# Kernel tuning notes

Hardware: AMD Instinct MI355X
Metric: run time of the kernel (lower is better)

## Reference

```python
import jax, jax.numpy as jnp
import numpy as np

N = 100000
E = 1600000
IN_DIM = 256
HID = 64


def setup_inputs() -> dict:
    key = jax.random.key(0)
    k1, k2, k3 = jax.random.split(key, 3)
    x = jax.random.normal(k1, (N, IN_DIM), dtype=jnp.float32)
    edge_index = jax.random.randint(k2, (2, E), 0, N, dtype=jnp.int64)
    # glorot-ish init for GCNConv weight, zero bias (PyG default)
    W = jax.random.normal(k3, (IN_DIM, HID), dtype=jnp.float32) * (1.0 / np.sqrt(IN_DIM))
    b = jnp.zeros((HID,), dtype=jnp.float32)
    return {"x": x, "edge_index": edge_index, "W": W, "b": b}


def reference(x, edge_index, W, b):
    # GCNConv: out = D^{-1/2} (A + I) D^{-1/2} (X W) + b
    n = x.shape[0]
    # add self-loops
    loop = jnp.arange(n, dtype=edge_index.dtype)
    src = jnp.concatenate([edge_index[0], loop])  # [E+N]
    dst = jnp.concatenate([edge_index[1], loop])  # [E+N]
    # degree of target nodes (incl. self-loops)
    deg = jax.ops.segment_sum(jnp.ones_like(dst, dtype=x.dtype), dst, num_segments=n)
    dinv = jnp.where(deg > 0, jax.lax.rsqrt(deg), 0.0)  # deg^{-1/2}, inf->0
    norm = dinv[src] * dinv[dst]  # [E+N]
    h = x @ W  # [N, HID] transform before aggregation
    msg = h[src] * norm[:, None]  # gather + scale, [E+N, HID]
    out = jax.ops.segment_sum(msg, dst, num_segments=n)  # scatter-add
    return out + b
```

## Files before the change

kernel.cpp:

```cpp
#include <hip/hip_runtime.h>

typedef float floatx4 __attribute__((ext_vector_type(4)));
typedef short s16x8 __attribute__((ext_vector_type(8)));

#define WG 256
#define NBUCK 512
#define BSH 8
#define EBLK 512
#define CAP 8192

__device__ inline unsigned pack_bf16_rne(float a, float b) {
    unsigned ua = __float_as_uint(a), ub = __float_as_uint(b);
    ua = (ua + 0x7FFFu + ((ua >> 16) & 1u)) >> 16;
    ub = (ub + 0x7FFFu + ((ub >> 16) & 1u)) >> 16;
    return ua | (ub << 16);
}

union FragU {
    unsigned u[4];
    uint4 q;
    s16x8 v;
};

__global__ __launch_bounds__(WG) void k_build(const void* __restrict__ ei, int* __restrict__ cursor,
                                              unsigned* __restrict__ ebuf, int E) {
    __shared__ int h[NBUCK];
    __shared__ int base[NBUCK];
    __shared__ int s32flag;
    const int t = threadIdx.x;
    if (t == 0) s32flag = 0;
    for (int i = t; i < NBUCK; i += WG) h[i] = 0;
    __syncthreads();
    {
        const int* w = (const int*)ei;
        int nz = 0;
        for (int j = t; j < 4096; j += WG) nz |= (w[2 * j + 1] != 0);
        if (nz) atomicOr(&s32flag, 1);
    }
    __syncthreads();
    const bool i32 = (s32flag != 0);
    const int chunk = (E + EBLK - 1) / EBLK;
    const int s = blockIdx.x * chunk;
    const int eend = min(E, s + chunk);
    if (i32) {
        const int* pd = (const int*)ei + E;
        for (int e = s + t; e < eend; e += WG) atomicAdd(&h[pd[e] >> BSH], 1);
    } else {
        const long long* pd = (const long long*)ei + E;
        for (int e = s + t; e < eend; e += WG) atomicAdd(&h[(int)pd[e] >> BSH], 1);
    }
    __syncthreads();
    for (int i = t; i < NBUCK; i += WG) {
        int c = h[i];
        base[i] = c ? atomicAdd(&cursor[i], c) : 0;
        h[i] = 0;
    }
    __syncthreads();
    for (int e = s + t; e < eend; e += WG) {
        int sN, dN;
        if (i32) {
            const int* p = (const int*)ei;
            sN = p[e];
            dN = p[E + e];
        } else {
            const long long* p = (const long long*)ei;
            sN = (int)p[e];
            dN = (int)p[(long long)E + e];
        }
        int bkt = dN >> BSH;
        int pos = base[bkt] + atomicAdd(&h[bkt], 1);
        if (pos < CAP) ebuf[(size_t)bkt * CAP + pos] = (unsigned)sN | ((unsigned)(dN & 255) << 24);
    }
}

__global__ __launch_bounds__(WG) void k_mid(const unsigned* __restrict__ ebuf, const int* __restrict__ cursor,
                                            int* __restrict__ off, int* __restrict__ srcs,
                                            float* __restrict__ dinv,
                                            const float* __restrict__ x, const float* __restrict__ W,
                                            unsigned short* __restrict__ g, int N, int nbuse) {
    __shared__ unsigned smem[2048 * 4];
    const int t = threadIdx.x;

    if ((int)blockIdx.x < nbuse) {
        int* red = (int*)smem;
        int* h = red + 256;
        int* sc = h + 256;
        int* cur = sc + 256;
        const int b = blockIdx.x;
        const int node0 = b << BSH;
        const int rows = min(256, N - node0);
        int part = 0;
        for (int i = t; i < b; i += WG) part += min(cursor[i], CAP);
        red[t] = part;
        h[t] = 0;
        __syncthreads();
        for (int d = WG / 2; d > 0; d >>= 1) {
            if (t < d) red[t] += red[t + d];
            __syncthreads();
        }
        const int ebase = red[0];
        const int cnt = min(cursor[b], CAP);
        const unsigned* eb = ebuf + (size_t)b * CAP;
        for (int j = t; j < cnt; j += WG) atomicAdd(&h[eb[j] >> 24], 1);
        __syncthreads();
        const int deg = (t < rows) ? h[t] + 1 : 0;
        sc[t] = deg;
        __syncthreads();
        for (int d = 1; d < 256; d <<= 1) {
            int a = (t >= d) ? sc[t - d] : 0;
            __syncthreads();
            sc[t] += a;
            __syncthreads();
        }
        const int basef = ebase + node0;
        const int local = sc[t] - deg;
        if (t < rows) {
            off[node0 + t] = basef + local;
            srcs[basef + local] = node0 + t;
            cur[t] = local + 1;
            dinv[node0 + t] = rsqrtf((float)deg);
        }
        if (b == nbuse - 1 && t == 0) off[N] = ebase + cnt + N;
        __syncthreads();
        for (int j = t; j < cnt; j += WG) {
            unsigned w = eb[j];
            int dl = (int)(w >> 24);
            int pos = basef + atomicAdd(&cur[dl], 1);
            srcs[pos] = (int)(w & 0xFFFFFFu);
        }
    } else {
        const int bb = blockIdx.x - nbuse;
        for (int q = t; q < 2048; q += WG) {
            const int kb = q >> 8, nt = (q >> 6) & 3, ln = q & 63;
            const int quad = ln >> 4, l15 = ln & 15;
            const int col = nt * 16 + l15;
            const int krow = kb * 32 + quad * 8;
            unsigned up[4];
#pragma unroll
            for (int p = 0; p < 4; p++) {
                float a = W[(krow + 2 * p) * 64 + col];
                float b2 = W[(krow + 2 * p + 1) * 64 + col];
                up[p] = pack_bf16_rne(a, b2);
            }
            uint4 pk = {up[0], up[1], up[2], up[3]};
            *(uint4*)(&smem[q * 4]) = pk;
        }
        __syncthreads();

        const int wv = t >> 6;
        const int lane = t & 63;
        const int quad = lane >> 4, l15 = lane & 15;

        long long arow = (long long)bb * 64 + wv * 16 + l15;
        if (arow >= N) arow = N - 1;
        const float* xr = x + arow * 256 + quad * 8;

        floatx4 xv[8][2];
#pragma unroll
        for (int kb = 0; kb < 8; kb++) {
            xv[kb][0] = *(const floatx4*)(xr + kb * 32);
            xv[kb][1] = *(const floatx4*)(xr + kb * 32 + 4);
        }

        floatx4 acc[4];
#pragma unroll
        for (int nt = 0; nt < 4; nt++) acc[nt] = 0.f;

#pragma unroll
        for (int kb = 0; kb < 8; kb++) {
            FragU a;
            a.u[0] = pack_bf16_rne(xv[kb][0][0], xv[kb][0][1]);
            a.u[1] = pack_bf16_rne(xv[kb][0][2], xv[kb][0][3]);
            a.u[2] = pack_bf16_rne(xv[kb][1][0], xv[kb][1][1]);
            a.u[3] = pack_bf16_rne(xv[kb][1][2], xv[kb][1][3]);
#pragma unroll
            for (int nt = 0; nt < 4; nt++) {
                FragU b2;
                b2.q = *(const uint4*)(&smem[((kb * 4 + nt) * 64 + lane) * 4]);
                acc[nt] = __builtin_amdgcn_mfma_f32_16x16x32_bf16(a.v, b2.v, acc[nt], 0, 0, 0);
            }
        }

        const long long orow0 = (long long)bb * 64 + wv * 16 + quad * 4;
#pragma unroll
        for (int r = 0; r < 4; r++) {
            const long long orow = orow0 + r;
            if (orow < N) {
#pragma unroll
                for (int nt = 0; nt < 4; nt++) {
                    float v = acc[nt][r];
                    unsigned uv = __float_as_uint(v);
                    uv = (uv + 0x7FFFu + ((uv >> 16) & 1u)) >> 16;
                    g[orow * 64 + nt * 16 + l15] = (unsigned short)uv;
                }
            }
        }
    }
}

__global__ __launch_bounds__(WG) void k_gather(const unsigned short* __restrict__ g,
                                               const int* __restrict__ off, const int* __restrict__ srcs,
                                               const float* __restrict__ dinv, const float* __restrict__ bias,
                                               float* __restrict__ out, int N) {
    int wid = (blockIdx.x * WG + threadIdx.x) >> 6;
    int lane = threadIdx.x & 63;
    if (wid >= N) return;
    int grp = lane >> 3;
    int c8 = (lane & 7) * 8;
    int e0 = off[wid], e1 = off[wid + 1];
    float a0 = 0.f, a1 = 0.f, a2 = 0.f, a3 = 0.f, a4 = 0.f, a5 = 0.f, a6 = 0.f, a7 = 0.f;
    int e = e0 + grp;
    int s = (e < e1) ? srcs[e] : 0;
    while (e < e1) {
        int en = e + 8;
        int sn = (en < e1) ? srcs[en] : 0;
        float ds = dinv[s];
        uint4 v = *(const uint4*)(g + (long long)s * 64 + c8);
        a0 += ds * __uint_as_float(v.x << 16);
        a1 += ds * __uint_as_float(v.x & 0xFFFF0000u);
        a2 += ds * __uint_as_float(v.y << 16);
        a3 += ds * __uint_as_float(v.y & 0xFFFF0000u);
        a4 += ds * __uint_as_float(v.z << 16);
        a5 += ds * __uint_as_float(v.z & 0xFFFF0000u);
        a6 += ds * __uint_as_float(v.w << 16);
        a7 += ds * __uint_as_float(v.w & 0xFFFF0000u);
        s = sn;
        e = en;
    }
#pragma unroll
    for (int m = 8; m <= 32; m <<= 1) {
        a0 += __shfl_xor(a0, m, 64);
        a1 += __shfl_xor(a1, m, 64);
        a2 += __shfl_xor(a2, m, 64);
        a3 += __shfl_xor(a3, m, 64);
        a4 += __shfl_xor(a4, m, 64);
        a5 += __shfl_xor(a5, m, 64);
        a6 += __shfl_xor(a6, m, 64);
        a7 += __shfl_xor(a7, m, 64);
    }
    if (grp == 0) {
        float d = dinv[wid];
        const floatx4 b0 = *(const floatx4*)(bias + c8);
        const floatx4 b1 = *(const floatx4*)(bias + c8 + 4);
        floatx4 o0, o1;
        o0[0] = d * a0 + b0[0];
        o0[1] = d * a1 + b0[1];
        o0[2] = d * a2 + b0[2];
        o0[3] = d * a3 + b0[3];
        o1[0] = d * a4 + b1[0];
        o1[1] = d * a5 + b1[1];
        o1[2] = d * a6 + b1[2];
        o1[3] = d * a7 + b1[3];
        *(floatx4*)(out + (long long)wid * 64 + c8) = o0;
        *(floatx4*)(out + (long long)wid * 64 + c8 + 4) = o1;
    }
}

extern "C" void kernel_launch(void* const* d_in, const int* in_sizes, int n_in,
                              void* d_out, int out_size, void* d_ws, size_t ws_size,
                              hipStream_t stream) {
    const float* x = (const float*)d_in[0];
    const void* ei = d_in[1];
    const float* W = (const float*)d_in[2];
    const float* b = (const float*)d_in[3];
    float* out = (float*)d_out;

    const int N = in_sizes[0] / 256;
    const int E = in_sizes[1] / 2;
    const int NBUSE = (N + 255) >> BSH;
    const int GEMMB = (N + 63) / 64;

    char* ws = (char*)d_ws;
    size_t o = 0;
    auto alloc = [&](size_t bytes) -> void* {
        void* p = ws + o;
        o += (bytes + 255) & ~(size_t)255;
        return p;
    };
    float* dinv = (float*)alloc((size_t)N * 4);
    unsigned short* g = (unsigned short*)alloc((size_t)N * 64 * 2);
    unsigned* ebuf = (unsigned*)alloc((size_t)NBUSE * CAP * 4);
    int* cursor = (int*)alloc((size_t)NBUCK * 4);
    int* off = (int*)alloc((size_t)(N + 1) * 4);
    int* srcs = (int*)alloc((size_t)(E + N) * 4);
    if (o > ws_size) return;

    hipMemsetAsync(cursor, 0, (size_t)NBUCK * 4, stream);
    k_build<<<EBLK, WG, 0, stream>>>(ei, cursor, ebuf, E);
    k_mid<<<NBUSE + GEMMB, WG, 0, stream>>>(ebuf, cursor, off, srcs, dinv, x, W, g, N, NBUSE);
    k_gather<<<(N * 64 + WG - 1) / WG, WG, 0, stream>>>(g, off, srcs, dinv, b, out, N);
}
```

Measured before the change: 269.3 us.

## Overlap edge bucketing with GEMM in one launch and pre-pack W once

```diff
diff --git a/kernel.cpp b/kernel.cpp
--- a/kernel.cpp
+++ b/kernel.cpp
@@ -16,134 +16,100 @@
     return ua | (ub << 16);
 }
 
+__device__ inline float bf_lo(unsigned u) { return __uint_as_float(u << 16); }
+__device__ inline float bf_hi(unsigned u) { return __uint_as_float(u & 0xFFFF0000u); }
+
 union FragU {
     unsigned u[4];
     uint4 q;
     s16x8 v;
 };
 
-__global__ __launch_bounds__(WG) void k_build(const void* __restrict__ ei, int* __restrict__ cursor,
-                                              unsigned* __restrict__ ebuf, int E) {
-    __shared__ int h[NBUCK];
-    __shared__ int base[NBUCK];
-    __shared__ int s32flag;
-    const int t = threadIdx.x;
-    if (t == 0) s32flag = 0;
-    for (int i = t; i < NBUCK; i += WG) h[i] = 0;
-    __syncthreads();
-    {
-        const int* w = (const int*)ei;
-        int nz = 0;
-        for (int j = t; j < 4096; j += WG) nz |= (w[2 * j + 1] != 0);
-        if (nz) atomicOr(&s32flag, 1);
-    }
-    __syncthreads();
-    const bool i32 = (s32flag != 0);
-    const int chunk = (E + EBLK - 1) / EBLK;
-    const int s = blockIdx.x * chunk;
-    const int eend = min(E, s + chunk);
-    if (i32) {
-        const int* pd = (const int*)ei + E;
-        for (int e = s + t; e < eend; e += WG) atomicAdd(&h[pd[e] >> BSH], 1);
-    } else {
-        const long long* pd = (const long long*)ei + E;
-        for (int e = s + t; e < eend; e += WG) atomicAdd(&h[(int)pd[e] >> BSH], 1);
-    }
-    __syncthreads();
-    for (int i = t; i < NBUCK; i += WG) {
-        int c = h[i];
-        base[i] = c ? atomicAdd(&cursor[i], c) : 0;
-        h[i] = 0;
-    }
-    __syncthreads();
-    for (int e = s + t; e < eend; e += WG) {
-        int sN, dN;
-        if (i32) {
-            const int* p = (const int*)ei;
-            sN = p[e];
-            dN = p[E + e];
-        } else {
-            const long long* p = (const long long*)ei;
-            sN = (int)p[e];
-            dN = (int)p[(long long)E + e];
-        }
-        int bkt = dN >> BSH;
-        int pos = base[bkt] + atomicAdd(&h[bkt], 1);
-        if (pos < CAP) ebuf[(size_t)bkt * CAP + pos] = (unsigned)sN | ((unsigned)(dN & 255) << 24);
-    }
-}
-
-__global__ __launch_bounds__(WG) void k_mid(const unsigned* __restrict__ ebuf, const int* __restrict__ cursor,
-                                            int* __restrict__ off, int* __restrict__ srcs,
-                                            float* __restrict__ dinv,
-                                            const float* __restrict__ x, const float* __restrict__ W,
-                                            unsigned short* __restrict__ g, int N, int nbuse) {
+__global__ __launch_bounds__(WG) void k_prep(const float* __restrict__ W, unsigned* __restrict__ Wf,
+                                             int* __restrict__ cursor) {
+    if (blockIdx.x == 0) {
+        if (threadIdx.x < NBUCK / 2) *(int2*)(cursor + threadIdx.x * 2) = {0, 0};
+    }
+    const int q = blockIdx.x * WG + threadIdx.x;
+    const int kb = q >> 8, nt = (q >> 6) & 3, ln = q & 63;
+    const int quad = ln >> 4, l15 = ln & 15;
+    const int col = nt * 16 + l15;
+    const int krow = kb * 32 + quad * 8;
+    unsigned up[4];
+#pragma unroll
+    for (int p = 0; p < 4; p++) {
+        float a = W[(krow + 2 * p) * 64 + col];
+        float b = W[(krow + 2 * p + 1) * 64 + col];
+        up[p] = pack_bf16_rne(a, b);
+    }
+    uint4 pk = {up[0], up[1], up[2], up[3]};
+    *(uint4*)(&Wf[q * 4]) = pk;
+}
+
+__global__ __launch_bounds__(WG) void k_bg(const void* __restrict__ ei, int* __restrict__ cursor,
+                                           unsigned* __restrict__ ebuf,
+                                           const float* __restrict__ x, const unsigned* __restrict__ Wf,
+                                           unsigned short* __restrict__ g, int N, int E) {
     __shared__ unsigned smem[2048 * 4];
     const int t = threadIdx.x;
-
-    if ((int)blockIdx.x < nbuse) {
-        int* red = (int*)smem;
-        int* h = red + 256;
-        int* sc = h + 256;
-        int* cur = sc + 256;
-        const int b = blockIdx.x;
-        const int node0 = b << BSH;
-        const int rows = min(256, N - node0);
-        int part = 0;
-        for (int i = t; i < b; i += WG) part += min(cursor[i], CAP);
-        red[t] = part;
-        h[t] = 0;
-        __syncthreads();
-        for (int d = WG / 2; d > 0; d >>= 1) {
-            if (t < d) red[t] += red[t + d];
-            __syncthreads();
-        }
-        const int ebase = red[0];
-        const int cnt = min(cursor[b], CAP);
-        const unsigned* eb = ebuf + (size_t)b * CAP;
-        for (int j = t; j < cnt; j += WG) atomicAdd(&h[eb[j] >> 24], 1);
-        __syncthreads();
-        const int deg = (t < rows) ? h[t] + 1 : 0;
-        sc[t] = deg;
-        __syncthreads();
-        for (int d = 1; d < 256; d <<= 1) {
-            int a = (t >= d) ? sc[t - d] : 0;
-            __syncthreads();
-            sc[t] += a;
-            __syncthreads();
-        }
-        const int basef = ebase + node0;
-        const int local = sc[t] - deg;
-        if (t < rows) {
-            off[node0 + t] = basef + local;
-            srcs[basef + local] = node0 + t;
-            cur[t] = local + 1;
-            dinv[node0 + t] = rsqrtf((float)deg);
-        }
-        if (b == nbuse - 1 && t == 0) off[N] = ebase + cnt + N;
-        __syncthreads();
-        for (int j = t; j < cnt; j += WG) {
-            unsigned w = eb[j];
-            int dl = (int)(w >> 24);
-            int pos = basef + atomicAdd(&cur[dl], 1);
-            srcs[pos] = (int)(w & 0xFFFFFFu);
+    const int b = blockIdx.x;
+    const bool isBuild = ((b & 3) == 0) && ((b >> 2) < EBLK);
+
+    if (isBuild) {
+        int* h = (int*)smem;
+        int* base = h + NBUCK;
+        int* s32flag = base + NBUCK;
+        const int bid = b >> 2;
+        if (t == 0) *s32flag = 0;
+        for (int i = t; i < NBUCK; i += WG) h[i] = 0;
+        __syncthreads();
+        {
+            const int* w = (const int*)ei;
+            int nz = 0;
+            for (int j = t; j < 4096; j += WG) nz |= (w[2 * j + 1] != 0);
+            if (nz) atomicOr(s32flag, 1);
+        }
+        __syncthreads();
+        const bool i32 = (*s32flag != 0);
+        const int chunk = (E + EBLK - 1) / EBLK;
+        const int s = bid * chunk;
+        const int eend = min(E, s + chunk);
+        if (i32) {
+            const int* pd = (const int*)ei + E;
+            for (int e = s + t; e < eend; e += WG) atomicAdd(&h[pd[e] >> BSH], 1);
+        } else {
+            const long long* pd = (const long long*)ei + E;
+            for (int e = s + t; e < eend; e += WG) atomicAdd(&h[(int)pd[e] >> BSH], 1);
+        }
+        __syncthreads();
+        for (int i = t; i < NBUCK; i += WG) {
+            int c = h[i];
+            base[i] = c ? atomicAdd(&cursor[i], c) : 0;
+            h[i] = 0;
+        }
+        __syncthreads();
+        for (int e = s + t; e < eend; e += WG) {
+            int sN, dN;
+            if (i32) {
+                const int* p = (const int*)ei;
+                sN = p[e];
+                dN = p[E + e];
+            } else {
+                const long long* p = (const long long*)ei;
+                sN = (int)p[e];
+                dN = (int)p[(long long)E + e];
+            }
+            int bkt = dN >> BSH;
+            int pos = base[bkt] + atomicAdd(&h[bkt], 1);
+            if (pos < CAP) ebuf[(size_t)bkt * CAP + pos] = (unsigned)sN | ((unsigned)(dN & 255) << 24);
         }
     } else {
-        const int bb = blockIdx.x - nbuse;
-        for (int q = t; q < 2048; q += WG) {
-            const int kb = q >> 8, nt = (q >> 6) & 3, ln = q & 63;
-            const int quad = ln >> 4, l15 = ln & 15;
-            const int col = nt * 16 + l15;
-            const int krow = kb * 32 + quad * 8;
-            unsigned up[4];
-#pragma unroll
-            for (int p = 0; p < 4; p++) {
-                float a = W[(krow + 2 * p) * 64 + col];
-                float b2 = W[(krow + 2 * p + 1) * 64 + col];
-                up[p] = pack_bf16_rne(a, b2);
-            }
-            uint4 pk = {up[0], up[1], up[2], up[3]};
-            *(uint4*)(&smem[q * 4]) = pk;
+        const int builds_before = min((b + 3) >> 2, EBLK);
+        const int bb = b - builds_before;
+        {
+            const uint4* src4 = (const uint4*)Wf;
+            uint4* dst4 = (uint4*)smem;
+            for (int q = t; q < 2048; q += WG) dst4[q] = src4[q];
         }
         __syncthreads();
 
@@ -195,6 +161,58 @@
                 }
             }
         }
+    }
+}
+
+__global__ __launch_bounds__(WG) void k_csr(const unsigned* __restrict__ ebuf, const int* __restrict__ cursor,
+                                            int* __restrict__ off, int* __restrict__ srcs,
+                                            float* __restrict__ dinv, int N, int nbuse) {
+    __shared__ int red[WG];
+    __shared__ int h[256];
+    __shared__ int sc[256];
+    __shared__ int cur[256];
+    const int t = threadIdx.x;
+    const int b = blockIdx.x;
+    const int node0 = b << BSH;
+    const int rows = min(256, N - node0);
+    int part = 0;
+    for (int i = t; i < b; i += WG) part += min(cursor[i], CAP);
+    red[t] = part;
+    h[t] = 0;
+    __syncthreads();
+    for (int d = WG / 2; d > 0; d >>= 1) {
+        if (t < d) red[t] += red[t + d];
+        __syncthreads();
+    }
+    const int ebase = red[0];
+    const int cnt = min(cursor[b], CAP);
+    const unsigned* eb = ebuf + (size_t)b * CAP;
+    for (int j = t; j < cnt; j += WG) atomicAdd(&h[eb[j] >> 24], 1);
+    __syncthreads();
+    const int deg = (t < rows) ? h[t] + 1 : 0;
+    sc[t] = deg;
+    __syncthreads();
+    for (int d = 1; d < 256; d <<= 1) {
+        int a = (t >= d) ? sc[t - d] : 0;
+        __syncthreads();
+        sc[t] += a;
+        __syncthreads();
+    }
+    const int basef = ebase + node0;
+    const int local = sc[t] - deg;
+    if (t < rows) {
+        off[node0 + t] = basef + local;
+        srcs[basef + local] = node0 + t;
+        cur[t] = local + 1;
+        dinv[node0 + t] = rsqrtf((float)deg);
+    }
+    if (b == nbuse - 1 && t == 0) off[N] = ebase + cnt + N;
+    __syncthreads();
+    for (int j = t; j < cnt; j += WG) {
+        unsigned w = eb[j];
+        int dl = (int)(w >> 24);
+        int pos = basef + atomicAdd(&cur[dl], 1);
+        srcs[pos] = (int)(w & 0xFFFFFFu);
     }
 }
 
@@ -211,20 +229,22 @@
     float a0 = 0.f, a1 = 0.f, a2 = 0.f, a3 = 0.f, a4 = 0.f, a5 = 0.f, a6 = 0.f, a7 = 0.f;
     int e = e0 + grp;
     int s = (e < e1) ? srcs[e] : 0;
+    float ds = dinv[s];
     while (e < e1) {
         int en = e + 8;
         int sn = (en < e1) ? srcs[en] : 0;
-        float ds = dinv[s];
+        float dsn = dinv[sn];
         uint4 v = *(const uint4*)(g + (long long)s * 64 + c8);
-        a0 += ds * __uint_as_float(v.x << 16);
-        a1 += ds * __uint_as_float(v.x & 0xFFFF0000u);
-        a2 += ds * __uint_as_float(v.y << 16);
-        a3 += ds * __uint_as_float(v.y & 0xFFFF0000u);
-        a4 += ds * __uint_as_float(v.z << 16);
-        a5 += ds * __uint_as_float(v.z & 0xFFFF0000u);
-        a6 += ds * __uint_as_float(v.w << 16);
-        a7 += ds * __uint_as_float(v.w & 0xFFFF0000u);
+        a0 += ds * bf_lo(v.x);
+        a1 += ds * bf_hi(v.x);
+        a2 += ds * bf_lo(v.y);
+        a3 += ds * bf_hi(v.y);
+        a4 += ds * bf_lo(v.z);
+        a5 += ds * bf_hi(v.z);
+        a6 += ds * bf_lo(v.w);
+        a7 += ds * bf_hi(v.w);
         s = sn;
+        ds = dsn;
         e = en;
     }
 #pragma unroll
@@ -281,12 +301,13 @@
     unsigned short* g = (unsigned short*)alloc((size_t)N * 64 * 2);
     unsigned* ebuf = (unsigned*)alloc((size_t)NBUSE * CAP * 4);
     int* cursor = (int*)alloc((size_t)NBUCK * 4);
+    unsigned* Wf = (unsigned*)alloc((size_t)2048 * 16);
     int* off = (int*)alloc((size_t)(N + 1) * 4);
     int* srcs = (int*)alloc((size_t)(E + N) * 4);
     if (o > ws_size) return;
 
-    hipMemsetAsync(cursor, 0, (size_t)NBUCK * 4, stream);
-    k_build<<<EBLK, WG, 0, stream>>>(ei, cursor, ebuf, E);
-    k_mid<<<NBUSE + GEMMB, WG, 0, stream>>>(ebuf, cursor, off, srcs, dinv, x, W, g, N, NBUSE);
+    k_prep<<<8, WG, 0, stream>>>(W, Wf, cursor);
+    k_bg<<<4 * EBLK + (GEMMB - 3 * EBLK), WG, 0, stream>>>(ei, cursor, ebuf, x, Wf, g, N, E);
+    k_csr<<<NBUSE, WG, 0, stream>>>(ebuf, cursor, off, srcs, dinv, N, NBUSE);
     k_gather<<<(N * 64 + WG - 1) / WG, WG, 0, stream>>>(g, off, srcs, dinv, b, out, N);
 }
```

Result: slower. 284.3 us (+5.6%).
